# Kernel optimization log

Measured on AMD Instinct MI355X. Metric: run time of the kernel, lower is better.

The kernel has to match this reference:

```python
import jax, jax.numpy as jnp
import numpy as np

KS = 3          # kernel_size
PAD = 1         # padding
N = KS * KS     # 9 sampling points
S2 = 2 ** 0.5
ANGLES = [0, 45, 90, 135, 180]

# angle-dependent extra offsets (x, y), indexed by angle // 45
_OFF = {
    0: ([0.0] * 9, [0.0] * 9),
    1: ([1 - S2, 1 - S2 * 0.5, 1, -S2 * 0.5, 0, S2 * 0.5, -1, S2 * 0.5 - 1, S2 - 1],
        [1, S2 * 0.5, S2 - 1, 1 - S2 * 0.5, 0, S2 * 0.5 - 1, 1 - S2, -S2 * 0.5, -1]),
    2: ([0, 1, 2, -1, 0, 1, -2, -1, 0],
        [2, 1, 0, 1, 0, -1, 0, -1, -2]),
    3: ([1, 1 + S2 * 0.5, 1 + S2, -S2 * 0.5, 0, S2 * 0.5, -1 - S2, -1 - S2 * 0.5, -1],
        [1 + S2, S2 * 0.5, -1, 1 + S2 * 0.5, 0, -1 - S2 * 0.5, 1, -S2 * 0.5, 1 + S2]),
    4: ([2, 2, 2, 0, 0, 0, -2, -2, -2],
        [2, 0, -2, 2, 0, -2, 2, 0, -2]),
}


def _deform_sample(x, angle):
    """Bilinear gather of the rotated 3x3 sampling grid -> (b,c,h*KS,w*KS)."""
    b, c, h, w = x.shape
    xp = jnp.pad(x, ((0, 0), (0, 0), (PAD, PAD), (PAD, PAD)))  # zero padding
    ph, pw = h + 2 * PAD, w + 2 * PAD

    ox_l, oy_l = _OFF[angle // 45]
    ox = jnp.asarray(np.array(ox_l, dtype=np.float32))
    oy = jnp.asarray(np.array(oy_l, dtype=np.float32))

    rng = np.arange(-(KS - 1) // 2, (KS - 1) // 2 + 1)
    pnx_np, pny_np = np.meshgrid(rng, rng, indexing='ij')  # torch default 'ij'
    pnx = jnp.asarray(pnx_np.reshape(-1).astype(np.float32))
    pny = jnp.asarray(pny_np.reshape(-1).astype(np.float32))

    # p = p_0 + p_n + offset ; keep x as (h,1,N) and y as (1,w,N), broadcast later
    px = jnp.arange(1, h + 1, dtype=jnp.float32)[:, None, None] + (pnx + ox)[None, None, :]  # (h,1,N)
    py = jnp.arange(1, w + 1, dtype=jnp.float32)[None, :, None] + (pny + oy)[None, None, :]  # (1,w,N)

    fx, fy = jnp.floor(px), jnp.floor(py)
    ql_x = jnp.clip(fx, 0, ph - 1)       # left-top row
    qr_x = jnp.clip(fx + 1, 0, ph - 1)   # right-bottom row
    ql_y = jnp.clip(fy, 0, pw - 1)
    qr_y = jnp.clip(fy + 1, 0, pw - 1)

    pxc = jnp.clip(px, 0, ph - 1)
    pyc = jnp.clip(py, 0, pw - 1)

    g_lt = (1 + (ql_x - pxc)) * (1 + (ql_y - pyc))  # (h,w,N) after broadcast
    g_rb = (1 - (qr_x - pxc)) * (1 - (qr_y - pyc))
    g_lb = (1 + (ql_x - pxc)) * (1 - (qr_y - pyc))
    g_rt = (1 - (qr_x - pxc)) * (1 + (ql_y - pyc))

    xf = xp.reshape(b, c, ph * pw)

    def gather(qx, qy):
        idx = qx.astype(jnp.int32) * pw + qy.astype(jnp.int32)      # (h,w,N)
        idx = jnp.broadcast_to(idx, (h, w, N)).reshape(-1)
        return jnp.take(xf, idx, axis=2).reshape(b, c, h, w, N)

    xo = (jnp.broadcast_to(g_lt, (h, w, N))[None, None] * gather(ql_x, ql_y)
          + jnp.broadcast_to(g_rb, (h, w, N))[None, None] * gather(qr_x, qr_y)
          + jnp.broadcast_to(g_lb, (h, w, N))[None, None] * gather(ql_x, qr_y)
          + jnp.broadcast_to(g_rt, (h, w, N))[None, None] * gather(qr_x, ql_y))

    # (b,c,h,w,N) -> (b,c,h*KS,w*KS) matching torch _reshape_x_offset
    xo = xo.reshape(b, c, h, w, KS, KS).transpose(0, 1, 2, 4, 3, 5).reshape(b, c, h * KS, w * KS)
    return xo


def _conv(xo, weight):
    # baseline_conv: stride=1, padding=0, no bias
    return jax.lax.conv_general_dilated(
        xo, weight, window_strides=(1, 1), padding='VALID',
        dimension_numbers=('NCHW', 'OIHW', 'NCHW'))


def setup_inputs() -> dict:
    key = jax.random.key(0)
    kx, kw = jax.random.split(key)
    x = jax.random.normal(kx, (2, 256, 64, 64), dtype=jnp.float32)
    weight = jax.random.normal(kw, (256, 256, 3, 3), dtype=jnp.float32) * 0.02
    return {"x": x, "weight": weight}


def reference(x, weight):
    return tuple(_conv(_deform_sample(x, a), weight) for a in ANGLES)
```

## Files before the change

### kernel.cpp

```cpp
#include <hip/hip_runtime.h>
#include <hip/hip_bf16.h>
#include <stdint.h>


#define S2F 1.41421356237309515f

__constant__ float c_ox[5][9] = {
  {0.f,0.f,0.f,0.f,0.f,0.f,0.f,0.f,0.f},
  {1.f-S2F, 1.f-S2F*0.5f, 1.f, -S2F*0.5f, 0.f, S2F*0.5f, -1.f, S2F*0.5f-1.f, S2F-1.f},
  {0.f,1.f,2.f,-1.f,0.f,1.f,-2.f,-1.f,0.f},
  {1.f, 1.f+S2F*0.5f, 1.f+S2F, -S2F*0.5f, 0.f, S2F*0.5f, -1.f-S2F, -1.f-S2F*0.5f, -1.f},
  {2.f,2.f,2.f,0.f,0.f,0.f,-2.f,-2.f,-2.f}
};
__constant__ float c_oy[5][9] = {
  {0.f,0.f,0.f,0.f,0.f,0.f,0.f,0.f,0.f},
  {1.f, S2F*0.5f, S2F-1.f, 1.f-S2F*0.5f, 0.f, S2F*0.5f-1.f, 1.f-S2F, -S2F*0.5f, -1.f},
  {2.f,1.f,0.f,1.f,0.f,-1.f,0.f,-1.f,-2.f},
  {1.f+S2F, S2F*0.5f, -1.f, 1.f+S2F*0.5f, 0.f, -1.f-S2F*0.5f, 1.f, -S2F*0.5f, 1.f+S2F},
  {2.f,0.f,-2.f,2.f,0.f,-2.f,2.f,0.f,-2.f}
};

typedef __bf16 bf16x8_t __attribute__((ext_vector_type(8)));
typedef float f32x4_t __attribute__((ext_vector_type(4)));

typedef const __attribute__((address_space(1))) void* as1cp;
typedef __attribute__((address_space(3))) void* as3p;

__device__ __forceinline__ void gload16(const void* g, void* l) {
  __builtin_amdgcn_global_load_lds((as1cp)g, (as3p)l, 16, 0, 0);
}

__global__ void k_transpose(const float* __restrict__ x, float* __restrict__ xT) {
  const int v = blockIdx.x, u = blockIdx.y, b = blockIdx.z;
  const int ic = threadIdx.x;
  xT[(((b*64 + u)*64 + v)*256) + ic] =
      x[(((b*256 + ic)*64 + u)*64) + v];
}

__global__ void k_wconv(const float* __restrict__ w, __hip_bfloat16* __restrict__ wb) {
  const int tid = blockIdx.x*256 + threadIdx.x;
  const int t = tid >> 16;
  const int rem = tid & 65535;
  const int oc = rem >> 8;
  const int ic = rem & 255;
  wb[tid] = __float2bfloat16(w[(oc*256 + ic)*9 + t]);
}

__global__ void k_sample(const float* __restrict__ xT,
                         __hip_bfloat16* __restrict__ xo, int a0)
{
  const int aidx = a0 + blockIdx.z;
  __hip_bfloat16* xoa = xo + (size_t)blockIdx.z * (2ull*192*192*256);

  const int tid = threadIdx.x;
  const int ic = (tid & 63) * 4;
  const int j = blockIdx.x*4 + (tid >> 6);
  const int i = blockIdx.y;

  const int a = i / 3, r = i - 3*a;
  const int bc = j / 3, s = j - 3*bc;
  const int n = r*3 + s;
  const float px = (float)(a + r) + c_ox[aidx][n];
  const float py = (float)(bc + s) + c_oy[aidx][n];
  const float fx = floorf(px), fy = floorf(py);
  const float pxc = fminf(fmaxf(px, 0.f), 65.f);
  const float pyc = fminf(fmaxf(py, 0.f), 65.f);
  const int qlx = (int)fminf(fmaxf(fx,      0.f), 65.f);
  const int qrx = (int)fminf(fmaxf(fx + 1.f, 0.f), 65.f);
  const int qly = (int)fminf(fmaxf(fy,      0.f), 65.f);
  const int qry = (int)fminf(fmaxf(fy + 1.f, 0.f), 65.f);
  const float wlx = 1.f + (float)qlx - pxc;
  const float wrx = 1.f - (float)qrx + pxc;
  const float wly = 1.f + (float)qly - pyc;
  const float wry = 1.f - (float)qry + pyc;
  const float glt = wlx*wly, grb = wrx*wry, glb = wlx*wry, grt = wrx*wly;

  const bool inxl = (qlx >= 1) && (qlx <= 64);
  const bool inxr = (qrx >= 1) && (qrx <= 64);
  const bool inyl = (qly >= 1) && (qly <= 64);
  const bool inyr = (qry >= 1) && (qry <= 64);

  const f32x4_t zero = (f32x4_t){0.f,0.f,0.f,0.f};
  #pragma unroll
  for (int b = 0; b < 2; ++b) {
    const float* xb = xT + (size_t)b * (64*64*256);
    f32x4_t vlt = (inxl && inyl) ? *(const f32x4_t*)&xb[((qlx-1)*64 + (qly-1))*256 + ic] : zero;
    f32x4_t vrb = (inxr && inyr) ? *(const f32x4_t*)&xb[((qrx-1)*64 + (qry-1))*256 + ic] : zero;
    f32x4_t vlb = (inxl && inyr) ? *(const f32x4_t*)&xb[((qlx-1)*64 + (qry-1))*256 + ic] : zero;
    f32x4_t vrt = (inxr && inyl) ? *(const f32x4_t*)&xb[((qrx-1)*64 + (qly-1))*256 + ic] : zero;
    ushort4 pk;
    float v0 = glt*vlt[0] + grb*vrb[0] + glb*vlb[0] + grt*vrt[0];
    float v1 = glt*vlt[1] + grb*vrb[1] + glb*vlb[1] + grt*vrt[1];
    float v2 = glt*vlt[2] + grb*vrb[2] + glb*vlb[2] + grt*vrt[2];
    float v3 = glt*vlt[3] + grb*vrb[3] + glb*vlb[3] + grt*vrt[3];
    pk.x = __hip_bfloat16_raw(__float2bfloat16(v0)).x;
    pk.y = __hip_bfloat16_raw(__float2bfloat16(v1)).x;
    pk.z = __hip_bfloat16_raw(__float2bfloat16(v2)).x;
    pk.w = __hip_bfloat16_raw(__float2bfloat16(v3)).x;
    *(ushort4*)&xoa[(((size_t)b*192 + i)*192 + j)*256 + ic] = pk;
  }
}

__global__ __launch_bounds__(256, 2) void k_conv(
    const __hip_bfloat16* __restrict__ xo,
    const __hip_bfloat16* __restrict__ wb,
    float* __restrict__ out)
{
  __shared__ __align__(16) char smem[66048];
  const int tid = threadIdx.x;

  const int f = blockIdx.x;
  const int T = gridDim.x & ~15;
  int pairI, nt;
  if (f < T) { pairI = (f >> 4)*8 + (f & 7); nt = (f >> 3) & 1; }
  else       { pairI = (T >> 1) + ((f - T) >> 1); nt = f & 1; }
  const int ct = pairI % 3;
  const int yz = pairI / 3;
  const int i0 = (yz % 95) * 2;
  const int z  = yz / 95;
  const int oc0 = nt * 128;
  const int j0 = ct * 64;

  const int q8   = tid >> 3;
  const int slot = tid & 7;
  const int wv   = tid >> 6;
  const int sw   = slot ^ (q8 & 7);

  const char* xob = (const char*)xo + (size_t)z * 18874368u;
  const char* wbc = (const char*)wb;

  int arow[4], acol[4], brow[4];
  #pragma unroll
  for (int p = 0; p < 4; ++p) {
    const int m = p*32 + q8;
    arow[p] = i0 + (m >> 6);
    acol[p] = j0 + (m & 63);
    brow[p] = oc0 + m;
  }

  f32x4_t acc[4][4];
  #pragma unroll
  for (int fm = 0; fm < 4; ++fm)
    #pragma unroll
    for (int fn = 0; fn < 4; ++fn)
      acc[fm][fn] = (f32x4_t){0.f, 0.f, 0.f, 0.f};

  const int lane = tid & 63;
  const int lrow = lane & 15;
  const int lk   = lane >> 4;
  const int wm   = wv >> 1;
  const int wn   = wv & 1;

  auto stage = [&](int kk, int cur) {
    const int icg = kk / 9;
    const int t   = kk - icg*9;
    const int ki = t / 3, kj = t - 3*ki;
    char* sa = smem + cur*16384 + wv*1024;
    char* sb = smem + 32768 + cur*16384 + wv*1024;
    #pragma unroll
    for (int p = 0; p < 4; ++p) {
      int col = acol[p] + kj; col = (col > 191) ? 191 : col;
      const char* ga = xob + (((arow[p] + ki)*192 + col)*256 + icg*64)*2 + sw*16;
      gload16(ga, sa + p*4096);
      const char* gb = wbc + ((t*256 + brow[p])*256 + icg*64)*2 + sw*16;
      gload16(gb, sb + p*4096);
    }
  };

  auto compute = [&](int cur) {
    const char* sa = smem + cur*16384;
    const char* sb = smem + 32768 + cur*16384;
    bf16x8_t af[4][2], bfr[4][2];
    #pragma unroll
    for (int fi = 0; fi < 4; ++fi) {
      const int m = wm*64 + fi*16 + lrow;
      const int n = wn*64 + fi*16 + lrow;
      #pragma unroll
      for (int ks = 0; ks < 2; ++ks) {
        af[fi][ks]  = *(const bf16x8_t*)(sa + m*128 + (((ks*4 + lk) ^ (m & 7)) * 16));
        bfr[fi][ks] = *(const bf16x8_t*)(sb + n*128 + (((ks*4 + lk) ^ (n & 7)) * 16));
      }
    }
    #pragma unroll
    for (int fm = 0; fm < 4; ++fm)
      #pragma unroll
      for (int fn = 0; fn < 4; ++fn)
        #pragma unroll
        for (int ks = 0; ks < 2; ++ks)
          acc[fm][fn] = __builtin_amdgcn_mfma_f32_16x16x32_bf16(
              af[fm][ks], bfr[fn][ks], acc[fm][fn], 0, 0, 0);
  };

  stage(0, 0);
  __syncthreads();
  for (int kk = 0; kk < 36; ++kk) {
    const int cur = kk & 1;
    if (kk < 35) stage(kk + 1, cur ^ 1);
    compute(cur);
    __syncthreads();
  }

  float* eps = (float*)smem;
  #pragma unroll
  for (int fm = 0; fm < 4; ++fm)
    #pragma unroll
    for (int fn = 0; fn < 4; ++fn)
      #pragma unroll
      for (int r = 0; r < 4; ++r)
        eps[(wn*64 + fn*16 + lrow)*129 + (wm*64 + fm*16 + lk*4 + r)] = acc[fm][fn][r];
  __syncthreads();

  float* outb = out + (size_t)z * 9241600u;
  #pragma unroll
  for (int pass = 0; pass < 16; ++pass) {
    const int ocw = pass*8 + (tid >> 5);
    const int m4  = (tid & 31) * 4;
    const int di  = m4 >> 6, jc = m4 & 63;
    const int i = i0 + di, j = j0 + jc;
    const float v0 = eps[ocw*129 + m4 + 0];
    const float v1 = eps[ocw*129 + m4 + 1];
    const float v2 = eps[ocw*129 + m4 + 2];
    const float v3 = eps[ocw*129 + m4 + 3];
    float* dst = outb + ((size_t)(oc0 + ocw)*190 + i)*190 + j;
    if (j + 3 < 190) {
      *(float2*)dst       = make_float2(v0, v1);
      *(float2*)(dst + 2) = make_float2(v2, v3);
    } else {
      if (j     < 190) dst[0] = v0;
      if (j + 1 < 190) dst[1] = v1;
      if (j + 2 < 190) dst[2] = v2;
      if (j + 3 < 190) dst[3] = v3;
    }
  }
}

extern "C" void kernel_launch(void* const* d_in, const int* in_sizes, int n_in,
                              void* d_out, int out_size, void* d_ws, size_t ws_size,
                              hipStream_t stream)
{
  const float* x = (const float*)d_in[0];
  const float* w = (const float*)d_in[1];
  float* out = (float*)d_out;

  char* ws = (char*)d_ws;
  float*          xT = (float*)ws;
  __hip_bfloat16* wb = (__hip_bfloat16*)(ws + 8388608);
  __hip_bfloat16* xo = (__hip_bfloat16*)(ws + 9568256);

  const bool merged = (ws_size >= 198311936ull);

  k_transpose<<<dim3(64, 64, 2), 256, 0, stream>>>(x, xT);
  k_wconv<<<2304, 256, 0, stream>>>(w, wb);

  if (merged) {
    k_sample<<<dim3(48, 192, 5), 256, 0, stream>>>(xT, xo, 0);
    k_conv<<<5700, 256, 0, stream>>>(xo, wb, out);
  } else {
    for (int aidx = 0; aidx < 5; ++aidx) {
      k_sample<<<dim3(48, 192, 1), 256, 0, stream>>>(xT, xo, aidx);
      k_conv<<<1140, 256, 0, stream>>>(xo, wb, out + (size_t)aidx * 18483200u);
    }
  }
}
```

Before: 540.8 us.

## Load conv weights directly into registers from a fragment-ordered layout, halve LDS

The weight prepack now writes bf16 weights in an MFMA-fragment order. The conv kernel reads B fragments straight from global memory into registers instead of staging them through LDS, which halves shared memory to allow 4 blocks per CU. The epilogue is reworked to write half the tile at a time through a smaller LDS buffer with contiguous float2 row stores. This trades LDS traffic and capacity for per-wave global/L2 weight reads each K step and a fully unrolled K loop with more register pressure.

After: 921.4 us. +70.4%, slower.

```diff
diff --git a/kernel.cpp b/kernel.cpp
--- a/kernel.cpp
+++ b/kernel.cpp
@@ -37,13 +37,15 @@
       x[(((b*256 + ic)*64 + u)*64) + v];
 }
 
-__global__ void k_wconv(const float* __restrict__ w, __hip_bfloat16* __restrict__ wb) {
-  const int tid = blockIdx.x*256 + threadIdx.x;
-  const int t = tid >> 16;
-  const int rem = tid & 65535;
-  const int oc = rem >> 8;
-  const int ic = rem & 255;
-  wb[tid] = __float2bfloat16(w[(oc*256 + ic)*9 + t]);
+__global__ void k_wconv3(const float* __restrict__ w, __hip_bfloat16* __restrict__ wb3) {
+  const int g = blockIdx.x*256 + threadIdx.x;
+  const int e   = g & 7;
+  const int oc  = (g >> 3) & 255;
+  const int ksq = (g >> 11) & 7;
+  const int icg = (g >> 14) & 3;
+  const int tap = g >> 16;
+  const int ic = icg*64 + ksq*8 + e;
+  wb3[g] = __float2bfloat16(w[(oc*256 + ic)*9 + tap]);
 }
 
 __global__ void k_sample(const float* __restrict__ xT,
@@ -101,12 +103,12 @@
   }
 }
 
-__global__ __launch_bounds__(256, 2) void k_conv(
+__global__ __launch_bounds__(256, 4) void k_conv(
     const __hip_bfloat16* __restrict__ xo,
-    const __hip_bfloat16* __restrict__ wb,
+    const __hip_bfloat16* __restrict__ wb3,
     float* __restrict__ out)
 {
-  __shared__ __align__(16) char smem[66048];
+  __shared__ __align__(16) char smem[33792];
   const int tid = threadIdx.x;
 
   const int f = blockIdx.x;
@@ -127,15 +129,14 @@
   const int sw   = slot ^ (q8 & 7);
 
   const char* xob = (const char*)xo + (size_t)z * 18874368u;
-  const char* wbc = (const char*)wb;
-
-  int arow[4], acol[4], brow[4];
+  const char* wbc = (const char*)wb3;
+
+  int arow[4], acol[4];
   #pragma unroll
   for (int p = 0; p < 4; ++p) {
     const int m = p*32 + q8;
     arow[p] = i0 + (m >> 6);
     acol[p] = j0 + (m & 63);
-    brow[p] = oc0 + m;
   }
 
   f32x4_t acc[4][4];
@@ -151,85 +152,92 @@
   const int wm   = wv >> 1;
   const int wn   = wv & 1;
 
+  const int bL = lk*4096 + (oc0 + wn*64 + lrow)*16;
+  const int aBase = (wm*64 + lrow)*128;
+  const int xor0 = ((lk    ) ^ (lrow & 7)) * 16;
+  const int xor1 = ((lk + 4) ^ (lrow & 7)) * 16;
+
   auto stage = [&](int kk, int cur) {
     const int icg = kk / 9;
     const int t   = kk - icg*9;
     const int ki = t / 3, kj = t - 3*ki;
     char* sa = smem + cur*16384 + wv*1024;
-    char* sb = smem + 32768 + cur*16384 + wv*1024;
     #pragma unroll
     for (int p = 0; p < 4; ++p) {
       int col = acol[p] + kj; col = (col > 191) ? 191 : col;
       const char* ga = xob + (((arow[p] + ki)*192 + col)*256 + icg*64)*2 + sw*16;
       gload16(ga, sa + p*4096);
-      const char* gb = wbc + ((t*256 + brow[p])*256 + icg*64)*2 + sw*16;
-      gload16(gb, sb + p*4096);
     }
   };
 
-  auto compute = [&](int cur) {
+  stage(0, 0);
+  __syncthreads();
+
+  #pragma unroll
+  for (int kk = 0; kk < 36; ++kk) {
+    const int cur = kk & 1;
+    const int icg = kk / 9;
+    const int t   = kk - icg*9;
+    const char* bbase = wbc + (t*4 + icg)*32768 + bL;
+
+    bf16x8_t bq0[4], bq1[4];
+    #pragma unroll
+    for (int nf = 0; nf < 4; ++nf)
+      bq0[nf] = *(const bf16x8_t*)(bbase + nf*256);
+    #pragma unroll
+    for (int nf = 0; nf < 4; ++nf)
+      bq1[nf] = *(const bf16x8_t*)(bbase + 16384 + nf*256);
+
+    if (kk < 35) stage(kk + 1, cur ^ 1);
+
     const char* sa = smem + cur*16384;
-    const char* sb = smem + 32768 + cur*16384;
-    bf16x8_t af[4][2], bfr[4][2];
-    #pragma unroll
-    for (int fi = 0; fi < 4; ++fi) {
-      const int m = wm*64 + fi*16 + lrow;
-      const int n = wn*64 + fi*16 + lrow;
-      #pragma unroll
-      for (int ks = 0; ks < 2; ++ks) {
-        af[fi][ks]  = *(const bf16x8_t*)(sa + m*128 + (((ks*4 + lk) ^ (m & 7)) * 16));
-        bfr[fi][ks] = *(const bf16x8_t*)(sb + n*128 + (((ks*4 + lk) ^ (n & 7)) * 16));
-      }
-    }
+    bf16x8_t af[4];
+    #pragma unroll
+    for (int fm = 0; fm < 4; ++fm)
+      af[fm] = *(const bf16x8_t*)(sa + aBase + fm*2048 + xor0);
     #pragma unroll
     for (int fm = 0; fm < 4; ++fm)
       #pragma unroll
       for (int fn = 0; fn < 4; ++fn)
+        acc[fm][fn] = __builtin_amdgcn_mfma_f32_16x16x32_bf16(
+            af[fm], bq0[fn], acc[fm][fn], 0, 0, 0);
+    #pragma unroll
+    for (int fm = 0; fm < 4; ++fm)
+      af[fm] = *(const bf16x8_t*)(sa + aBase + fm*2048 + xor1);
+    #pragma unroll
+    for (int fm = 0; fm < 4; ++fm)
+      #pragma unroll
+      for (int fn = 0; fn < 4; ++fn)
+        acc[fm][fn] = __builtin_amdgcn_mfma_f32_16x16x32_bf16(
+            af[fm], bq1[fn], acc[fm][fn], 0, 0, 0);
+    __syncthreads();
+  }
+
+  float* eps = (float*)smem;
+  float* outb = out + (size_t)z * 9241600u;
+  const int ocr = tid >> 2, q = tid & 3;
+  const int iS = i0 + (q >> 1);
+  const int jb = j0 + (q & 1)*32;
+  const int kmax = (ct == 2 && (q & 1)) ? 30 : 32;
+
+  #pragma unroll
+  for (int h = 0; h < 2; ++h) {
+    __syncthreads();
+    if (wn == h) {
+      #pragma unroll
+      for (int fm = 0; fm < 4; ++fm)
         #pragma unroll
-        for (int ks = 0; ks < 2; ++ks)
-          acc[fm][fn] = __builtin_amdgcn_mfma_f32_16x16x32_bf16(
-              af[fm][ks], bfr[fn][ks], acc[fm][fn], 0, 0, 0);
-  };
-
-  stage(0, 0);
-  __syncthreads();
-  for (int kk = 0; kk < 36; ++kk) {
-    const int cur = kk & 1;
-    if (kk < 35) stage(kk + 1, cur ^ 1);
-    compute(cur);
+        for (int fn = 0; fn < 4; ++fn)
+          #pragma unroll
+          for (int r = 0; r < 4; ++r)
+            eps[(fn*16 + lrow)*132 + wm*64 + fm*16 + lk*4 + r] = acc[fm][fn][r];
+    }
     __syncthreads();
-  }
-
-  float* eps = (float*)smem;
-  #pragma unroll
-  for (int fm = 0; fm < 4; ++fm)
-    #pragma unroll
-    for (int fn = 0; fn < 4; ++fn)
-      #pragma unroll
-      for (int r = 0; r < 4; ++r)
-        eps[(wn*64 + fn*16 + lrow)*129 + (wm*64 + fm*16 + lk*4 + r)] = acc[fm][fn][r];
-  __syncthreads();
-
-  float* outb = out + (size_t)z * 9241600u;
-  #pragma unroll
-  for (int pass = 0; pass < 16; ++pass) {
-    const int ocw = pass*8 + (tid >> 5);
-    const int m4  = (tid & 31) * 4;
-    const int di  = m4 >> 6, jc = m4 & 63;
-    const int i = i0 + di, j = j0 + jc;
-    const float v0 = eps[ocw*129 + m4 + 0];
-    const float v1 = eps[ocw*129 + m4 + 1];
-    const float v2 = eps[ocw*129 + m4 + 2];
-    const float v3 = eps[ocw*129 + m4 + 3];
-    float* dst = outb + ((size_t)(oc0 + ocw)*190 + i)*190 + j;
-    if (j + 3 < 190) {
-      *(float2*)dst       = make_float2(v0, v1);
-      *(float2*)(dst + 2) = make_float2(v2, v3);
-    } else {
-      if (j     < 190) dst[0] = v0;
-      if (j + 1 < 190) dst[1] = v1;
-      if (j + 2 < 190) dst[2] = v2;
-      if (j + 3 < 190) dst[3] = v3;
+    {
+      float* dst = outb + (size_t)(oc0 + h*64 + ocr)*36100u + iS*190 + jb;
+      const float* src = eps + ocr*132 + q*32;
+      for (int k = 0; k < kmax; k += 2)
+        *(float2*)(dst + k) = make_float2(src[k], src[k + 1]);
     }
   }
 }
@@ -243,22 +251,22 @@
   float* out = (float*)d_out;
 
   char* ws = (char*)d_ws;
-  float*          xT = (float*)ws;
-  __hip_bfloat16* wb = (__hip_bfloat16*)(ws + 8388608);
-  __hip_bfloat16* xo = (__hip_bfloat16*)(ws + 9568256);
+  float*          xT  = (float*)ws;
+  __hip_bfloat16* wb3 = (__hip_bfloat16*)(ws + 8388608);
+  __hip_bfloat16* xo  = (__hip_bfloat16*)(ws + 9568256);
 
   const bool merged = (ws_size >= 198311936ull);
 
   k_transpose<<<dim3(64, 64, 2), 256, 0, stream>>>(x, xT);
-  k_wconv<<<2304, 256, 0, stream>>>(w, wb);
+  k_wconv3<<<2304, 256, 0, stream>>>(w, wb3);
 
   if (merged) {
     k_sample<<<dim3(48, 192, 5), 256, 0, stream>>>(xT, xo, 0);
-    k_conv<<<5700, 256, 0, stream>>>(xo, wb, out);
+    k_conv<<<5700, 256, 0, stream>>>(xo, wb3, out);
   } else {
     for (int aidx = 0; aidx < 5; ++aidx) {
       k_sample<<<dim3(48, 192, 1), 256, 0, stream>>>(xT, xo, aidx);
-      k_conv<<<1140, 256, 0, stream>>>(xo, wb, out + (size_t)aidx * 18483200u);
-    }
-  }
-}
+      k_conv<<<1140, 256, 0, stream>>>(xo, wb3, out + (size_t)aidx * 18483200u);
+    }
+  }
+}
```
